# Kernel optimization log

Measured on AMD Instinct MI355X. Metric: run time of the kernel, lower is better.

## Reference

```python
import jax, jax.numpy as jnp
import numpy as np

B, C, N = 2, 29, 8192
S, K = 1024, 16  # npoint, nsample
D = C + 3


def fps(xyz_t, npoint):
    # xyz_t: [B, N, 3] -> indices [B, npoint] (furthest point sampling, starts at idx 0)
    b, n, _ = xyz_t.shape

    def step(carry, _):
        dists, farthest = carry  # [B,N], [B]
        centroid = jnp.take_along_axis(xyz_t, farthest[:, None, None], axis=1)  # [B,1,3]
        d = jnp.sum((xyz_t - centroid) ** 2, axis=-1)  # [B,N]
        dists = jnp.minimum(dists, d)
        nxt = jnp.argmax(dists, axis=-1)
        return (dists, nxt), farthest

    init = (jnp.full((b, n), 1e10, xyz_t.dtype), jnp.zeros((b,), jnp.int32))
    _, idx = jax.lax.scan(step, init, None, length=npoint)
    return jnp.transpose(idx)  # [B, npoint]


def knn_self(pts, k):
    # pts: [B, S, 3] -> k nearest neighbor indices within the same set, [B, S, k]
    sq = jnp.sum(pts * pts, axis=-1)
    d2 = sq[:, :, None] + sq[:, None, :] - 2.0 * jnp.einsum('bic,bjc->bij', pts, pts)
    _, idx = jax.lax.top_k(-d2, k)
    return idx


def group(arr, idx):
    # arr: [B, C, N], idx: [B, S, K] -> [B, C, S, K]
    return jax.vmap(lambda a, i: a[:, i])(arr, idx)


def squeeze_2x2(x):
    # RealNVP alt-order squeeze: [n, c, h, w] -> [n, 4c, h/2, w/2]
    tl = x[:, :, 0::2, 0::2]
    br = x[:, :, 1::2, 1::2]
    tr = x[:, :, 0::2, 1::2]
    bl = x[:, :, 1::2, 0::2]
    return jnp.concatenate([tl, br, tr, bl], axis=1)


def conv2d(x, w):
    return jax.lax.conv_general_dilated(
        x, w, window_strides=(1, 1), padding='VALID',
        dimension_numbers=('NCHW', 'OIHW', 'NCHW'))


def setup_inputs() -> dict:
    key = jax.random.key(0)
    ks = jax.random.split(key, 6)
    return {
        'xyz': jax.random.normal(ks[0], (B, 3, N), jnp.float32),
        'feats': jax.random.normal(ks[1], (B, C, N), jnp.float32),
        'w0': jax.random.normal(ks[2], (64, 2 * D * 4, 3, 3), jnp.float32) * 0.02,
        'w1': jax.random.normal(ks[3], (64, 64, 3, 3), jnp.float32) * 0.02,
        'w2': jax.random.normal(ks[4], (128, 64, 3, 3), jnp.float32) * 0.02,
        'w3': jax.random.normal(ks[5], (128, 128, 2, 2), jnp.float32) * 0.02,
    }


def reference(xyz, feats, w0, w1, w2, w3):
    b, c, n = feats.shape
    xyz_t = jnp.transpose(xyz, (0, 2, 1))  # [B,N,3]
    fps_idx = fps(xyz_t, S)  # [B,S]
    new_xyz = jnp.take_along_axis(xyz, fps_idx[:, None, :], axis=2)  # [B,3,S]
    new_xyz_t = jnp.transpose(new_xyz, (0, 2, 1))  # [B,S,3]
    idx = knn_self(new_xyz_t, K)  # [B,S,K], values in [0,S)

    pos_grouped = group(new_xyz, idx)  # [B,3,S,K]
    feats_grouped = group(feats, idx)  # [B,C,S,K] (indices < S, as in original)
    pos_diff = pos_grouped - new_xyz[:, :, :, None]
    fg = jnp.concatenate([pos_diff, feats_grouped], axis=1)  # [B,D,S,K]

    # pairwise outer-product features; second half ([fg;1] x [fg;1] upper block) is all ones
    outer = jnp.einsum('bdsi,bdsj->bdsij', fg, fg)  # [B,D,S,K,K]
    mat = jnp.concatenate([outer, jnp.ones_like(outer)], axis=1)  # [B,2D,S,K,K]
    mat = jnp.transpose(mat, (0, 2, 1, 3, 4)).reshape(b * S, 2 * D, K, K)
    mat = squeeze_2x2(mat)  # [B*S, 8D, K/2, K/2]

    for w in (w0, w1, w2, w3):  # use_bn=False -> Identity bns; spatial 8->6->4->2->1
        mat = jax.nn.relu(conv2d(mat, w))

    new_points = jnp.transpose(mat.reshape(b, S, -1), (0, 2, 1))  # [B,128,S]
    return new_xyz, new_points, fps_idx
```

## Files before the change

kernel.cpp:

```cpp
#include <hip/hip_runtime.h>
#include <hip/hip_bf16.h>

#pragma clang fp contract(off)

#define NPTS 8192
#define NS   1024
#define NB   2
#define NC   29
#define NK   16


__global__ __launch_bounds__(256) void prep_kernel(
    const float* __restrict__ w0, const float* __restrict__ w1,
    const float* __restrict__ w2, const float* __restrict__ w3,
    float* __restrict__ w0t, float* __restrict__ w1t,
    float* __restrict__ w2t, float* __restrict__ w3t,
    float* __restrict__ bias0)
{
    int i = blockIdx.x * 256 + threadIdx.x;
    int n = gridDim.x * 256;
    for (int e = i; e < 73728; e += n) {
        int o = e & 63, r = e >> 6, tap = r % 9, ic2 = r / 9;
        int ic = ((ic2 >> 5) << 6) + (ic2 & 31);
        w0t[e] = w0[(o * 256 + ic) * 9 + tap];
    }
    for (int e = i; e < 36864; e += n) {
        int o = e & 63, r = e >> 6, tap = r % 9, ic = r / 9;
        w1t[e] = w1[(o * 64 + ic) * 9 + tap];
    }
    for (int e = i; e < 73728; e += n) {
        int o = e & 127, r = e >> 7, tap = r % 9, ic = r / 9;
        w2t[e] = w2[(o * 64 + ic) * 9 + tap];
    }
    for (int e = i; e < 65536; e += n) {
        int o = e & 127, r = e >> 7, tap = r & 3, ic = r >> 2;
        w3t[e] = w3[(o * 128 + ic) * 4 + tap];
    }
    if (i < 64) {
        float sum = 0.0f;
        for (int q = 0; q < 4; ++q)
            for (int c = 0; c < 32; ++c)
                for (int t = 0; t < 9; ++t)
                    sum += w0[(i * 256 + q * 64 + 32 + c) * 9 + t];
        bias0[i] = sum;
    }
}

__device__ __forceinline__ float wave_max_nonneg(float x) {
    int v = __float_as_int(x);
    int t;
    t = __builtin_amdgcn_update_dpp(0, v, 0x111, 0xf, 0xf, true);
    v = __float_as_int(fmaxf(__int_as_float(v), __int_as_float(t)));
    t = __builtin_amdgcn_update_dpp(0, v, 0x112, 0xf, 0xf, true);
    v = __float_as_int(fmaxf(__int_as_float(v), __int_as_float(t)));
    t = __builtin_amdgcn_update_dpp(0, v, 0x114, 0xf, 0xf, true);
    v = __float_as_int(fmaxf(__int_as_float(v), __int_as_float(t)));
    t = __builtin_amdgcn_update_dpp(0, v, 0x118, 0xf, 0xf, true);
    v = __float_as_int(fmaxf(__int_as_float(v), __int_as_float(t)));
    t = __builtin_amdgcn_update_dpp(0, v, 0x142, 0xa, 0xf, true);
    v = __float_as_int(fmaxf(__int_as_float(v), __int_as_float(t)));
    t = __builtin_amdgcn_update_dpp(0, v, 0x143, 0xc, 0xf, true);
    v = __float_as_int(fmaxf(__int_as_float(v), __int_as_float(t)));
    return __int_as_float(__builtin_amdgcn_readlane(v, 63));
}

__global__ __launch_bounds__(1024) void fps_kernel(
    const float* __restrict__ xyz,
    float* __restrict__ nx_ws, float* __restrict__ out)
{
    int b = blockIdx.x;
    int tid = threadIdx.x;
    const float* X = xyz + b * 3 * NPTS;

    __shared__ unsigned s_max[2];
    __shared__ int s_gi[2];
    __shared__ int s_idx[NS];

    float px[8], py[8], pz[8], dist[8];
#pragma unroll
    for (int i = 0; i < 8; ++i) {
        int gi = i * 1024 + tid;
        px[i] = X[gi];
        py[i] = X[NPTS + gi];
        pz[i] = X[2 * NPTS + gi];
        dist[i] = 1e10f;
    }

    float* out_fps = out + 268288 + b * NS;
    if (tid == 0) {
        s_idx[0] = 0; out_fps[0] = 0.0f;
        s_max[0] = 0u; s_max[1] = 0u;
        s_gi[0] = 0x7fffffff; s_gi[1] = 0x7fffffff;
    }
    __syncthreads();

    float cx = X[0], cy = X[NPTS], cz = X[2 * NPTS];
    int lane = tid & 63;

    for (int it = 1; it < NS; ++it) {
        int par = it & 1;
#pragma unroll
        for (int i = 0; i < 8; ++i) {
            float dx = px[i] - cx, dy = py[i] - cy, dz = pz[i] - cz;
            float d = (dx * dx + dy * dy) + dz * dz;
            dist[i] = fminf(dist[i], d);
        }
        float m0 = fmaxf(dist[0], dist[1]);
        float m1 = fmaxf(dist[2], dist[3]);
        float m2 = fmaxf(dist[4], dist[5]);
        float m3 = fmaxf(dist[6], dist[7]);
        float m4 = fmaxf(m0, m1);
        float m5 = fmaxf(m2, m3);
        float bv = fmaxf(m4, m5);
        float wm = wave_max_nonneg(bv);
        if (lane == 0) atomicMax(&s_max[par], __float_as_uint(wm));
        __syncthreads();
        float gbv = __uint_as_float(s_max[par]);
        if (tid == 0) { s_max[par ^ 1] = 0u; s_gi[par ^ 1] = 0x7fffffff; }
        if (bv == gbv) {
            int gi = 0;
#pragma unroll
            for (int i = 7; i >= 0; --i)
                if (dist[i] == gbv) gi = (i << 10) + tid;
            atomicMin(&s_gi[par], gi);
        }
        __syncthreads();
        int idx = s_gi[par];
        if (tid == 0) { out_fps[it] = (float)idx; s_idx[it] = idx; }
        cx = X[idx]; cy = X[NPTS + idx]; cz = X[2 * NPTS + idx];
    }
    __syncthreads();
    {
        int j = s_idx[tid];
        float x = X[j], y = X[NPTS + j], z = X[2 * NPTS + j];
        nx_ws[(b * 3 + 0) * NS + tid] = x; out[(b * 3 + 0) * NS + tid] = x;
        nx_ws[(b * 3 + 1) * NS + tid] = y; out[(b * 3 + 1) * NS + tid] = y;
        nx_ws[(b * 3 + 2) * NS + tid] = z; out[(b * 3 + 2) * NS + tid] = z;
    }
}

__global__ __launch_bounds__(256) void knn_kernel(
    const float* __restrict__ nx_ws, int* __restrict__ knn_ws)
{
    int q = blockIdx.x * 4 + (threadIdx.x >> 6);
    int lane = threadIdx.x & 63;
    int b = q >> 10, s = q & 1023;
    const float* P = nx_ws + b * 3 * NS;
    float qx = P[s], qy = P[NS + s], qz = P[2 * NS + s];
    float sqq = (qx * qx + qy * qy) + qz * qz;
    int base_j = lane * 16;
    float d2[16];
    {
        const float4* x4 = (const float4*)(P + base_j);
        const float4* y4 = (const float4*)(P + NS + base_j);
        const float4* z4 = (const float4*)(P + 2 * NS + base_j);
#pragma unroll
        for (int t = 0; t < 4; ++t) {
            float4 xv = x4[t], yv = y4[t], zv = z4[t];
            float xs[4] = { xv.x, xv.y, xv.z, xv.w };
            float ys[4] = { yv.x, yv.y, yv.z, yv.w };
            float zs[4] = { zv.x, zv.y, zv.z, zv.w };
#pragma unroll
            for (int e = 0; e < 4; ++e) {
                float xj = xs[e], yj = ys[e], zj = zs[e];
                float sqj = (xj * xj + yj * yj) + zj * zj;
                float dot = (qx * xj + qy * yj) + qz * zj;
                d2[t * 4 + e] = (sqq + sqj) - 2.0f * dot;
            }
        }
    }
    for (int r = 0; r < NK; ++r) {
        float lv = 3.0e38f; int li = 0;
#pragma unroll
        for (int i = 0; i < 16; ++i) { if (d2[i] < lv) { lv = d2[i]; li = i; } }
        int gj = base_j + li;
#pragma unroll
        for (int off = 32; off > 0; off >>= 1) {
            float ov = __shfl_xor(lv, off, 64);
            int   oj = __shfl_xor(gj, off, 64);
            if (ov < lv || (ov == lv && oj < gj)) { lv = ov; gj = oj; }
        }
        if (lane == 0) knn_ws[q * NK + r] = gj;
        if ((gj >> 4) == lane) {
            int li2 = gj & 15;
#pragma unroll
            for (int i = 0; i < 16; ++i) if (i == li2) d2[i] = 3.0e38f;
        }
    }
}

template<int GODD>
__device__ __forceinline__ void conv0_accum(
    const float* __restrict__ x0r, const float* __restrict__ wbase, float acc[9])
{
    for (int ic2 = 0; ic2 < 128; ++ic2) {
        const float4* x4 = (const float4*)(x0r + ic2 * 64);
        float rr[32];
#pragma unroll
        for (int j = 0; j < 4; ++j) {
            float4 t0 = x4[j * 2], t1 = x4[j * 2 + 1];
            rr[j*8+0]=t0.x; rr[j*8+1]=t0.y; rr[j*8+2]=t0.z; rr[j*8+3]=t0.w;
            rr[j*8+4]=t1.x; rr[j*8+5]=t1.y; rr[j*8+6]=t1.z; rr[j*8+7]=t1.w;
        }
        float w[9];
#pragma unroll
        for (int t = 0; t < 9; ++t) w[t] = wbase[(ic2 * 9 + t) * 64];
#pragma unroll
        for (int pp = 0; pp < 9; ++pp) {
            const int ly = GODD ? (pp < 3 ? 0 : 1) : (pp < 6 ? 0 : 1);
            const int xx = GODD ? (pp < 3 ? pp + 3 : pp - 3) : (pp < 6 ? pp : pp - 6);
#pragma unroll
            for (int ky = 0; ky < 3; ++ky)
#pragma unroll
                for (int kx = 0; kx < 3; ++kx)
                    acc[pp] = __builtin_fmaf(w[ky * 3 + kx], rr[(ly + ky) * 8 + xx + kx], acc[pp]);
        }
    }
}

__global__ __launch_bounds__(256) void conv_kernel(
    const float* __restrict__ feats, const float* __restrict__ nx_ws,
    const int* __restrict__ knn_ws,
    const float* __restrict__ w0t, const float* __restrict__ bias0,
    const float* __restrict__ w1t, const float* __restrict__ w2t,
    const float* __restrict__ w3t, float* __restrict__ out)
{
    __shared__ float s_fg[512];
    __shared__ int   s_ni[16];
    __shared__ float s_x0[8192];
    __shared__ float s_a1[64 * 36];
    __shared__ float s_a2[64 * 16];
    __shared__ float s_a3[128 * 4];

    int bs = blockIdx.x, b = bs >> 10, s = bs & 1023;
    int tid = threadIdx.x;
    if (tid < 16) s_ni[tid] = knn_ws[bs * NK + tid];
    __syncthreads();
    const float* P = nx_ws + b * 3 * NS;
#pragma unroll
    for (int e = tid; e < 512; e += 256) {
        int d = e >> 4, k = e & 15; int j = s_ni[k];
        float v = (d < 3) ? (P[d * NS + j] - P[d * NS + s])
                          : feats[(b * NC + (d - 3)) * NPTS + j];
        s_fg[e] = v;
    }
    __syncthreads();
    for (int e = tid; e < 8192; e += 256) {
        int ic2 = e >> 6, pos = e & 63, u = pos >> 3, v = pos & 7;
        int q = ic2 >> 5, ch = ic2 & 31;
        int ro = q & 1, co = ((q + 1) >> 1) & 1;
        s_x0[e] = s_fg[ch * 16 + 2 * u + ro] * s_fg[ch * 16 + 2 * v + co];
    }
    __syncthreads();

    int o = tid & 63, g = tid >> 6;
    {
        int r0 = g + (g >> 1);
        float acc[9];
        float bz = bias0[o];
#pragma unroll
        for (int p = 0; p < 9; ++p) acc[p] = bz;
        const float* x0r = s_x0 + r0 * 8;
        const float* wb = w0t + o;
        if (g & 1) conv0_accum<1>(x0r, wb, acc);
        else       conv0_accum<0>(x0r, wb, acc);
#pragma unroll
        for (int pp = 0; pp < 9; ++pp) s_a1[o * 36 + g * 9 + pp] = fmaxf(acc[pp], 0.0f);
    }
    __syncthreads();
    {
        float a[4] = {0, 0, 0, 0};
        const float* wb = w1t + o;
        for (int ic = 0; ic < 64; ++ic) {
            const float2* ar2 = (const float2*)(s_a1 + ic * 36 + g * 6);
            float r[18];
#pragma unroll
            for (int t = 0; t < 9; ++t) { float2 tv = ar2[t]; r[t*2] = tv.x; r[t*2+1] = tv.y; }
            float w[9];
#pragma unroll
            for (int t = 0; t < 9; ++t) w[t] = wb[(ic * 9 + t) * 64];
#pragma unroll
            for (int x = 0; x < 4; ++x)
#pragma unroll
                for (int ky = 0; ky < 3; ++ky)
#pragma unroll
                    for (int kx = 0; kx < 3; ++kx)
                        a[x] = __builtin_fmaf(w[ky * 3 + kx], r[ky * 6 + x + kx], a[x]);
        }
#pragma unroll
        for (int x = 0; x < 4; ++x) s_a2[o * 16 + g * 4 + x] = fmaxf(a[x], 0.0f);
    }
    __syncthreads();
    {
        int o2 = tid & 127, g2 = tid >> 7;
        float a[2] = {0, 0};
        const float* wb = w2t + o2;
        for (int ic = 0; ic < 64; ++ic) {
            const float4* ar4 = (const float4*)(s_a2 + ic * 16 + g2 * 4);
            float r[12];
#pragma unroll
            for (int t = 0; t < 3; ++t) { float4 tv = ar4[t]; r[t*4]=tv.x; r[t*4+1]=tv.y; r[t*4+2]=tv.z; r[t*4+3]=tv.w; }
            float w[9];
#pragma unroll
            for (int t = 0; t < 9; ++t) w[t] = wb[(ic * 9 + t) * 128];
#pragma unroll
            for (int x = 0; x < 2; ++x)
#pragma unroll
                for (int ky = 0; ky < 3; ++ky)
#pragma unroll
                    for (int kx = 0; kx < 3; ++kx)
                        a[x] = __builtin_fmaf(w[ky * 3 + kx], r[ky * 4 + x + kx], a[x]);
        }
#pragma unroll
        for (int x = 0; x < 2; ++x) s_a3[o2 * 4 + g2 * 2 + x] = fmaxf(a[x], 0.0f);
    }
    __syncthreads();
    if (tid < 128) {
        float acc = 0.0f;
        const float* wb = w3t + tid;
        for (int ic = 0; ic < 128; ++ic) {
            float4 av = *(const float4*)(s_a3 + ic * 4);
            float wa = wb[(ic * 4 + 0) * 128];
            float wbv = wb[(ic * 4 + 1) * 128];
            float wc = wb[(ic * 4 + 2) * 128];
            float wd = wb[(ic * 4 + 3) * 128];
            acc = __builtin_fmaf(wa, av.x, acc);
            acc = __builtin_fmaf(wbv, av.y, acc);
            acc = __builtin_fmaf(wc, av.z, acc);
            acc = __builtin_fmaf(wd, av.w, acc);
        }
        out[6144 + (b * 128 + tid) * NS + s] = fmaxf(acc, 0.0f);
    }
}

extern "C" void kernel_launch(void* const* d_in, const int* in_sizes, int n_in,
                              void* d_out, int out_size, void* d_ws, size_t ws_size,
                              hipStream_t stream) {
    const float* xyz   = (const float*)d_in[0];
    const float* feats = (const float*)d_in[1];
    const float* w0    = (const float*)d_in[2];
    const float* w1    = (const float*)d_in[3];
    const float* w2    = (const float*)d_in[4];
    const float* w3    = (const float*)d_in[5];
    float* out = (float*)d_out;

    char* ws = (char*)d_ws;
    float* nx_ws  = (float*)(ws + 8192);
    int*   knn_ws = (int*)(ws + 32768);
    float* w0t    = (float*)(ws + 163840);
    float* bias0  = (float*)(ws + 458752);
    float* w1t    = (float*)(ws + 459008);
    float* w2t    = (float*)(ws + 606464);
    float* w3t    = (float*)(ws + 901376);

    prep_kernel<<<128, 256, 0, stream>>>(w0, w1, w2, w3, w0t, w1t, w2t, w3t, bias0);
    fps_kernel<<<NB, 1024, 0, stream>>>(xyz, nx_ws, out);
    knn_kernel<<<(NB * NS) / 4, 256, 0, stream>>>(nx_ws, knn_ws);
    conv_kernel<<<NB * NS, 256, 0, stream>>>(feats, nx_ws, knn_ws, w0t, bias0, w1t, w2t, w3t, out);
}
```

Baseline: 1.441 ms.

## Rework FPS loop with packed 64-bit argmax key and one barrier per step

```diff
diff --git a/kernel.cpp b/kernel.cpp
--- a/kernel.cpp
+++ b/kernel.cpp
@@ -64,7 +64,12 @@
     return __int_as_float(__builtin_amdgcn_readlane(v, 63));
 }
 
-__global__ __launch_bounds__(1024) void fps_kernel(
+__device__ __forceinline__ float2 sub2(float2 a, float2 b){ return make_float2(a.x-b.x, a.y-b.y); }
+__device__ __forceinline__ float2 mul2(float2 a, float2 b){ return make_float2(a.x*b.x, a.y*b.y); }
+__device__ __forceinline__ float2 add2(float2 a, float2 b){ return make_float2(a.x+b.x, a.y+b.y); }
+__device__ __forceinline__ float2 min2(float2 a, float2 b){ return make_float2(fminf(a.x,b.x), fminf(a.y,b.y)); }
+
+__global__ __launch_bounds__(512, 1) void fps_kernel(
     const float* __restrict__ xyz,
     float* __restrict__ nx_ws, float* __restrict__ out)
 {
@@ -72,70 +77,69 @@
     int tid = threadIdx.x;
     const float* X = xyz + b * 3 * NPTS;
 
-    __shared__ unsigned s_max[2];
-    __shared__ int s_gi[2];
+    __shared__ unsigned long long s_key[4];
     __shared__ int s_idx[NS];
 
-    float px[8], py[8], pz[8], dist[8];
-#pragma unroll
-    for (int i = 0; i < 8; ++i) {
-        int gi = i * 1024 + tid;
-        px[i] = X[gi];
-        py[i] = X[NPTS + gi];
-        pz[i] = X[2 * NPTS + gi];
-        dist[i] = 1e10f;
-    }
-
+    float2 px[8], py[8], pz[8], dist[8];
+#pragma unroll
+    for (int j = 0; j < 8; ++j) {
+        int g0 = (2 * j) * 512 + tid;
+        px[j] = make_float2(X[g0],            X[g0 + 512]);
+        py[j] = make_float2(X[NPTS + g0],     X[NPTS + g0 + 512]);
+        pz[j] = make_float2(X[2*NPTS + g0],   X[2*NPTS + g0 + 512]);
+        dist[j] = make_float2(1e10f, 1e10f);
+    }
+
+    if (tid < 4) s_key[tid] = 0ull;
+    if (tid == 0) s_idx[0] = 0;
+    __syncthreads();
+
+    float cx = X[0], cy = X[NPTS], cz = X[2 * NPTS];
+
+    for (int it = 1; it < NS; ++it) {
+        float2 c2x = make_float2(cx, cx), c2y = make_float2(cy, cy), c2z = make_float2(cz, cz);
+        float pm[8];
+#pragma unroll
+        for (int j = 0; j < 8; ++j) {
+            float2 dx = sub2(px[j], c2x), dy = sub2(py[j], c2y), dz = sub2(pz[j], c2z);
+            float2 d = add2(add2(mul2(dx, dx), mul2(dy, dy)), mul2(dz, dz));
+            float2 nd = min2(dist[j], d);
+            dist[j] = nd;
+            pm[j] = fmaxf(nd.x, nd.y);
+        }
+        float q0 = fmaxf(pm[0], pm[1]), q1 = fmaxf(pm[2], pm[3]);
+        float q2 = fmaxf(pm[4], pm[5]), q3 = fmaxf(pm[6], pm[7]);
+        float bv = fmaxf(fmaxf(q0, q1), fmaxf(q2, q3));
+        float wm = wave_max_nonneg(bv);
+        if (bv == wm) {
+            int jj = 0;
+#pragma unroll
+            for (int j = 7; j >= 0; --j) if (pm[j] == wm) jj = j;
+            int i2 = 2 * jj + ((dist[jj].x == wm) ? 0 : 1);
+            int gi = (i2 << 9) + tid;
+            unsigned long long key =
+                ((unsigned long long)__float_as_uint(wm) << 32) | (unsigned)(8191 - gi);
+            atomicMax(&s_key[it & 3], key);
+        }
+        __syncthreads();
+        unsigned long long k = s_key[it & 3];
+        int idx = 8191 - (int)(unsigned)(k & 0xffffffffull);
+        if (tid == 0) {
+            s_idx[it] = idx;
+            s_key[(it + 2) & 3] = 0ull;
+        }
+        int u = __builtin_amdgcn_readfirstlane(idx);
+        cx = X[u]; cy = X[NPTS + u]; cz = X[2 * NPTS + u];
+    }
+    __syncthreads();
     float* out_fps = out + 268288 + b * NS;
-    if (tid == 0) {
-        s_idx[0] = 0; out_fps[0] = 0.0f;
-        s_max[0] = 0u; s_max[1] = 0u;
-        s_gi[0] = 0x7fffffff; s_gi[1] = 0x7fffffff;
-    }
-    __syncthreads();
-
-    float cx = X[0], cy = X[NPTS], cz = X[2 * NPTS];
-    int lane = tid & 63;
-
-    for (int it = 1; it < NS; ++it) {
-        int par = it & 1;
-#pragma unroll
-        for (int i = 0; i < 8; ++i) {
-            float dx = px[i] - cx, dy = py[i] - cy, dz = pz[i] - cz;
-            float d = (dx * dx + dy * dy) + dz * dz;
-            dist[i] = fminf(dist[i], d);
-        }
-        float m0 = fmaxf(dist[0], dist[1]);
-        float m1 = fmaxf(dist[2], dist[3]);
-        float m2 = fmaxf(dist[4], dist[5]);
-        float m3 = fmaxf(dist[6], dist[7]);
-        float m4 = fmaxf(m0, m1);
-        float m5 = fmaxf(m2, m3);
-        float bv = fmaxf(m4, m5);
-        float wm = wave_max_nonneg(bv);
-        if (lane == 0) atomicMax(&s_max[par], __float_as_uint(wm));
-        __syncthreads();
-        float gbv = __uint_as_float(s_max[par]);
-        if (tid == 0) { s_max[par ^ 1] = 0u; s_gi[par ^ 1] = 0x7fffffff; }
-        if (bv == gbv) {
-            int gi = 0;
-#pragma unroll
-            for (int i = 7; i >= 0; --i)
-                if (dist[i] == gbv) gi = (i << 10) + tid;
-            atomicMin(&s_gi[par], gi);
-        }
-        __syncthreads();
-        int idx = s_gi[par];
-        if (tid == 0) { out_fps[it] = (float)idx; s_idx[it] = idx; }
-        cx = X[idx]; cy = X[NPTS + idx]; cz = X[2 * NPTS + idx];
-    }
-    __syncthreads();
-    {
-        int j = s_idx[tid];
+    for (int s = tid; s < NS; s += 512) {
+        int j = s_idx[s];
+        out_fps[s] = (float)j;
         float x = X[j], y = X[NPTS + j], z = X[2 * NPTS + j];
-        nx_ws[(b * 3 + 0) * NS + tid] = x; out[(b * 3 + 0) * NS + tid] = x;
-        nx_ws[(b * 3 + 1) * NS + tid] = y; out[(b * 3 + 1) * NS + tid] = y;
-        nx_ws[(b * 3 + 2) * NS + tid] = z; out[(b * 3 + 2) * NS + tid] = z;
+        nx_ws[(b * 3 + 0) * NS + s] = x; out[(b * 3 + 0) * NS + s] = x;
+        nx_ws[(b * 3 + 1) * NS + s] = y; out[(b * 3 + 1) * NS + s] = y;
+        nx_ws[(b * 3 + 2) * NS + s] = z; out[(b * 3 + 2) * NS + s] = z;
     }
 }
 
@@ -354,7 +358,7 @@
     float* w3t    = (float*)(ws + 901376);
 
     prep_kernel<<<128, 256, 0, stream>>>(w0, w1, w2, w3, w0t, w1t, w2t, w3t, bias0);
-    fps_kernel<<<NB, 1024, 0, stream>>>(xyz, nx_ws, out);
+    fps_kernel<<<NB, 512, 0, stream>>>(xyz, nx_ws, out);
     knn_kernel<<<(NB * NS) / 4, 256, 0, stream>>>(nx_ws, knn_ws);
     conv_kernel<<<NB * NS, 256, 0, stream>>>(feats, nx_ws, knn_ws, w0t, bias0, w1t, w2t, w3t, out);
 }
```

New measurement: 1.530 ms. 6.2% more time.
